# Kernel tuning notes

Hardware: AMD Instinct MI355X
Metric: run time of the kernel (lower is better)

Reference implementation:

```python
import jax, jax.numpy as jnp
import numpy as np

B, T = 32768, 32
OBJ_V, PRED_V = 179, 46
E_OBJ, E_PRED, H = 5, 5, 32
IN_DIM = E_OBJ + E_PRED + 2 + 4  # 16, matches LSTMCell input size


def setup_inputs() -> dict:
    key = jax.random.key(0)
    ks = jax.random.split(key, 12)
    s = 0.1
    return {
        "input_objects": jax.random.randint(ks[0], (B, T), 0, OBJ_V),
        "input_boxes": jax.random.uniform(ks[1], (B, T, 4), dtype=jnp.float32),
        "predicates": jax.random.randint(ks[2], (B, T), 0, PRED_V),
        "subject_indicators": jax.random.randint(ks[3], (B, T), 0, 2),
        "target_object": jax.random.randint(ks[4], (B,), 0, OBJ_V),
        "obj_emb": jax.random.normal(ks[5], (OBJ_V, E_OBJ), dtype=jnp.float32) * s,
        "pred_emb": jax.random.normal(ks[6], (PRED_V, E_PRED), dtype=jnp.float32) * s,
        "W_ih": jax.random.normal(ks[7], (4 * H, IN_DIM), dtype=jnp.float32) * s,
        "W_hh": jax.random.normal(ks[8], (4 * H, H), dtype=jnp.float32) * s,
        "b_ih": jnp.zeros((4 * H,), dtype=jnp.float32),
        "b_hh": jnp.zeros((4 * H,), dtype=jnp.float32),
        "fc2_W": jax.random.normal(ks[9], (4, H), dtype=jnp.float32) * s,
        "fc2_b": jnp.zeros((4,), dtype=jnp.float32),
    }


def _forward(input_objects, input_boxes, predicates, subject_indicators,
             obj_emb, pred_emb, W_ih, W_hh, b_ih, b_hh, fc2_W, fc2_b):
    # concatenate_features, vectorized over all timesteps at once: [B,T,16]
    feats = jnp.concatenate([
        obj_emb[input_objects],                                   # [B,T,5]
        pred_emb[predicates],                                     # [B,T,5]
        jax.nn.one_hot(subject_indicators, 2, dtype=jnp.float32), # [B,T,2]
        input_boxes,                                              # [B,T,4]
    ], axis=-1)
    xs = jnp.transpose(feats, (1, 0, 2))  # [T,B,16] for scan over time

    def step(carry, x):
        h, c = carry
        gates = x @ W_ih.T + b_ih + h @ W_hh.T + b_hh  # [B,4H]
        i, f, g, o = jnp.split(gates, 4, axis=-1)      # torch gate order i,f,g,o
        i = jax.nn.sigmoid(i)
        f = jax.nn.sigmoid(f)
        g = jnp.tanh(g)
        o = jax.nn.sigmoid(o)
        c = f * c + i * g
        h = o * jnp.tanh(c)
        return (h, c), None

    h0 = jnp.zeros((input_objects.shape[0], H), dtype=jnp.float32)
    (h, _), _ = jax.lax.scan(step, (h0, h0), xs)
    out = h @ fc2_W.T + fc2_b          # output_fc2 on last hidden state
    return jnp.clip(out, 0.0, 1.0)     # torch.clamp(min=0, max=1)


def reference(input_objects, input_boxes, predicates, subject_indicators, target_object,
              obj_emb, pred_emb, W_ih, W_hh, b_ih, b_hh, fc2_W, fc2_b):
    # target_object is accepted by the torch forward but unused in its body
    return _forward(input_objects, input_boxes, predicates, subject_indicators,
                    obj_emb, pred_emb, W_ih, W_hh, b_ih, b_hh, fc2_W, fc2_b)
```

## Files before the change

### kernel.cpp

```cpp
#include <hip/hip_runtime.h>

#define LDS_BYTES 17952

typedef _Float16 f16x8 __attribute__((ext_vector_type(8)));
typedef float    f32x4 __attribute__((ext_vector_type(4)));

#define LOG2E     1.44269504088896f
#define TWO_LOG2E 2.88539008177793f

__device__ __forceinline__ float sig_pre(float a) {
    return __builtin_amdgcn_rcpf(1.0f + __builtin_amdgcn_exp2f(a));
}
__device__ __forceinline__ float tanh_pre(float a) {
    return 1.0f - 2.0f * __builtin_amdgcn_rcpf(1.0f + __builtin_amdgcn_exp2f(a));
}

__global__ __launch_bounds__(64, 2)
void lstm_fused(const int* __restrict__ objs,
                const float* __restrict__ boxes,
                const int* __restrict__ preds,
                const int* __restrict__ subj,
                const float* __restrict__ obj_emb,
                const float* __restrict__ pred_emb,
                const float* __restrict__ W_ih,
                const float* __restrict__ W_hh,
                const float* __restrict__ b_ih,
                const float* __restrict__ b_hh,
                const float* __restrict__ fc2_W,
                const float* __restrict__ fc2_b,
                float* __restrict__ out)
{
    extern __shared__ char smem[];
    const int tid  = threadIdx.x;
    const int quad = tid >> 4;
    const int cidx = tid & 15;
    const int XOFF = 0, HOFF = 16640, ZOFF = 17920;

    {
        int* z = (int*)(smem + HOFF);
        #pragma unroll
        for (int i = 0; i < 6; ++i) {
            int idx = tid + i * 64;
            if (idx < 328) z[idx] = 0;
        }
    }

    {
        int b  = tid >> 2;
        int t0 = (tid & 3) << 3;
        long gb = (long)blockIdx.x * 16 + b;
        const int* op = objs  + gb * 32 + t0;
        const int* pp = preds + gb * 32 + t0;
        const int* sp = subj  + gb * 32 + t0;
        #pragma unroll
        for (int c = 0; c < 8; c += 4) {
            int4 ov = *(const int4*)(op + c);
            int4 pv = *(const int4*)(pp + c);
            int4 sv = *(const int4*)(sp + c);
            int oarr[4] = {ov.x, ov.y, ov.z, ov.w};
            int parr[4] = {pv.x, pv.y, pv.z, pv.w};
            int sarr[4] = {sv.x, sv.y, sv.z, sv.w};
            #pragma unroll
            for (int tt = 0; tt < 4; ++tt) {
                int t = t0 + c + tt;
                const float* eo = obj_emb  + oarr[tt] * 5;
                const float* ep = pred_emb + parr[tt] * 5;
                float4 bx = *(const float4*)(boxes + (gb * 32 + t) * 4);
                f16x8 lo, hi;
                lo[0]=(_Float16)eo[0]; lo[1]=(_Float16)eo[1]; lo[2]=(_Float16)eo[2];
                lo[3]=(_Float16)eo[3]; lo[4]=(_Float16)eo[4];
                lo[5]=(_Float16)ep[0]; lo[6]=(_Float16)ep[1]; lo[7]=(_Float16)ep[2];
                hi[0]=(_Float16)ep[3]; hi[1]=(_Float16)ep[4];
                hi[2]=(_Float16)(sarr[tt]==0 ? 1.0f : 0.0f);
                hi[3]=(_Float16)(sarr[tt]==1 ? 1.0f : 0.0f);
                hi[4]=(_Float16)bx.x; hi[5]=(_Float16)bx.y;
                hi[6]=(_Float16)bx.z; hi[7]=(_Float16)bx.w;
                char* dst = smem + XOFF + b * 1040 + t * 32;
                *(f16x8*)dst        = lo;
                *(f16x8*)(dst + 16) = hi;
            }
        }
    }

    f16x8 Wf[8][2];
    f32x4 bias4[8];
    #pragma unroll
    for (int j = 0; j < 8; ++j) {
        int n = j * 16 + cidx;
        float scale = (j >= 4 && j < 6) ? TWO_LOG2E : -LOG2E;
        float bv = (b_ih[n] + b_hh[n]) * scale;
        bias4[j] = (f32x4){bv, bv, bv, bv};
        #pragma unroll
        for (int ks = 0; ks < 2; ++ks) {
            f16x8 v;
            #pragma unroll
            for (int jj = 0; jj < 8; ++jj) {
                int k = ks * 32 + quad * 8 + jj;
                float val = (k < 16) ? W_ih[n * 16 + k]
                          : (k < 48) ? W_hh[n * 32 + (k - 16)]
                          : 0.0f;
                v[jj] = (_Float16)(val * scale);
            }
            Wf[j][ks] = v;
        }
    }

    const bool isx  = (quad < 2);
    int addr0 = isx ? (XOFF + cidx * 1040 + quad * 16)
                    : (HOFF + cidx * 80 + (quad - 2) * 16);
    const int inc0  = isx ? 32 : 0;
    const int addr1 = isx ? (HOFF + cidx * 80 + 32 + quad * 16)
                          : ZOFF;
    const int wr_b  = quad * 4;

    float cst[8] = {0,0,0,0,0,0,0,0};
    float hl[8];

    __syncthreads();

    #pragma unroll 4
    for (int t = 0; t < 32; ++t) {
        f16x8 a0 = *(const f16x8*)(smem + addr0);
        f16x8 a1 = *(const f16x8*)(smem + addr1);
        addr0 += inc0;

        f32x4 acc[8];
        #pragma unroll
        for (int j = 0; j < 8; ++j) {
            f32x4 a = __builtin_amdgcn_mfma_f32_16x16x32_f16(a0, Wf[j][0], bias4[j], 0, 0, 0);
            acc[j]  = __builtin_amdgcn_mfma_f32_16x16x32_f16(a1, Wf[j][1], a, 0, 0, 0);
        }

        #pragma unroll
        for (int r = 0; r < 4; ++r) {
            float si0 = sig_pre(acc[0][r]);
            float si1 = sig_pre(acc[1][r]);
            float sf0 = sig_pre(acc[2][r]);
            float sf1 = sig_pre(acc[3][r]);
            float tg0 = tanh_pre(acc[4][r]);
            float tg1 = tanh_pre(acc[5][r]);
            float so0 = sig_pre(acc[6][r]);
            float so1 = sig_pre(acc[7][r]);
            float c0 = fmaf(sf0, cst[2*r],   si0 * tg0);
            float c1 = fmaf(sf1, cst[2*r+1], si1 * tg1);
            cst[2*r] = c0; cst[2*r+1] = c1;
            float h0 = so0 * tanh_pre(c0 * TWO_LOG2E);
            float h1 = so1 * tanh_pre(c1 * TWO_LOG2E);
            hl[2*r] = h0; hl[2*r+1] = h1;
            *(_Float16*)(smem + HOFF + (wr_b + r) * 80 + cidx * 2)      = (_Float16)h0;
            *(_Float16*)(smem + HOFF + (wr_b + r) * 80 + 32 + cidx * 2) = (_Float16)h1;
        }
    }

    __syncthreads();
    #pragma unroll
    for (int r = 0; r < 4; ++r) {
        *(float*)(smem + (wr_b + r) * 144 + cidx * 4)      = hl[2*r];
        *(float*)(smem + (wr_b + r) * 144 + 64 + cidx * 4) = hl[2*r+1];
    }
    __syncthreads();

    {
        int b = tid >> 2, jj = tid & 3;
        const float* fw   = fc2_W + jj * 32;
        const float* hrow = (const float*)(smem + b * 144);
        float s = fc2_b[jj];
        #pragma unroll
        for (int k = 0; k < 8; ++k) {
            float4 hv = *(const float4*)(hrow + k * 4);
            s += fw[k*4+0] * hv.x + fw[k*4+1] * hv.y
               + fw[k*4+2] * hv.z + fw[k*4+3] * hv.w;
        }
        s = fminf(fmaxf(s, 0.0f), 1.0f);
        out[(long)blockIdx.x * 64 + tid] = s;
    }
}

extern "C" void kernel_launch(void* const* d_in, const int* in_sizes, int n_in,
                              void* d_out, int out_size, void* d_ws, size_t ws_size,
                              hipStream_t stream)
{
    lstm_fused<<<2048, 64, LDS_BYTES, stream>>>(
        (const int*)d_in[0], (const float*)d_in[1], (const int*)d_in[2],
        (const int*)d_in[3],
        (const float*)d_in[5], (const float*)d_in[6],
        (const float*)d_in[7], (const float*)d_in[8],
        (const float*)d_in[9], (const float*)d_in[10],
        (const float*)d_in[11], (const float*)d_in[12],
        (float*)d_out);
}
```

Baseline: 154.8 us.

## Pass hidden state via ds_bpermute and precompute input-gate MFMA one step ahead

The recurrent LSTM loop no longer round-trips the hidden state through LDS. Each step packs h into fp16 pairs and redistributes them across lanes with ds_bpermute, with the MFMA operands swapped (W as A, activations as B) so the output layout matches. The input-projection MFMA for step t+1 is issued right after the gate math, off the h-dependent critical path, and the recurrent step needs only one MFMA per gate block instead of two. This adds eight bpermutes per step and some selects, and changes the K layout of the weights.

```diff
diff --git a/kernel.cpp b/kernel.cpp
--- a/kernel.cpp
+++ b/kernel.cpp
@@ -1,6 +1,6 @@
 #include <hip/hip_runtime.h>
 
-#define LDS_BYTES 17952
+#define LDS_BYTES 16656
 
 typedef _Float16 f16x8 __attribute__((ext_vector_type(8)));
 typedef float    f32x4 __attribute__((ext_vector_type(4)));
@@ -13,6 +13,11 @@
 }
 __device__ __forceinline__ float tanh_pre(float a) {
     return 1.0f - 2.0f * __builtin_amdgcn_rcpf(1.0f + __builtin_amdgcn_exp2f(a));
+}
+__device__ __forceinline__ int pack2(float a, float b) {
+    union { _Float16 h[2]; int i; } u;
+    u.h[0] = (_Float16)a; u.h[1] = (_Float16)b;
+    return u.i;
 }
 
 __global__ __launch_bounds__(64, 2)
@@ -34,16 +39,9 @@
     const int tid  = threadIdx.x;
     const int quad = tid >> 4;
     const int cidx = tid & 15;
-    const int XOFF = 0, HOFF = 16640, ZOFF = 17920;
-
-    {
-        int* z = (int*)(smem + HOFF);
-        #pragma unroll
-        for (int i = 0; i < 6; ++i) {
-            int idx = tid + i * 64;
-            if (idx < 328) z[idx] = 0;
-        }
-    }
+    const int XOFF = 0, ZOFF = 16640;
+
+    if (tid < 4) ((int*)(smem + ZOFF))[tid] = 0;
 
     {
         int b  = tid >> 2;
@@ -86,10 +84,8 @@
     f32x4 bias4[8];
     #pragma unroll
     for (int j = 0; j < 8; ++j) {
+        float scale = (j == 4 || j == 5) ? TWO_LOG2E : -LOG2E;
         int n = j * 16 + cidx;
-        float scale = (j >= 4 && j < 6) ? TWO_LOG2E : -LOG2E;
-        float bv = (b_ih[n] + b_hh[n]) * scale;
-        bias4[j] = (f32x4){bv, bv, bv, bv};
         #pragma unroll
         for (int ks = 0; ks < 2; ++ks) {
             f16x8 v;
@@ -97,39 +93,59 @@
             for (int jj = 0; jj < 8; ++jj) {
                 int k = ks * 32 + quad * 8 + jj;
                 float val = (k < 16) ? W_ih[n * 16 + k]
-                          : (k < 48) ? W_hh[n * 32 + (k - 16)]
+                          : (k >= 32) ? W_hh[n * 32 + (k - 32)]
                           : 0.0f;
                 v[jj] = (_Float16)(val * scale);
             }
             Wf[j][ks] = v;
         }
-    }
-
-    const bool isx  = (quad < 2);
-    int addr0 = isx ? (XOFF + cidx * 1040 + quad * 16)
-                    : (HOFF + cidx * 80 + (quad - 2) * 16);
-    const int inc0  = isx ? 32 : 0;
-    const int addr1 = isx ? (HOFF + cidx * 80 + 32 + quad * 16)
-                          : ZOFF;
-    const int wr_b  = quad * 4;
-
+        #pragma unroll
+        for (int r = 0; r < 4; ++r) {
+            int nr = j * 16 + quad * 4 + r;
+            bias4[j][r] = (b_ih[nr] + b_hh[nr]) * scale;
+        }
+    }
+
+    const bool qlow = (quad < 2);
+    int       xaddr = qlow ? (XOFF + cidx * 1040 + quad * 16) : ZOFF;
+    const int xinc  = qlow ? 32 : 0;
+    const int idx_lo = (((quad & 1) << 5) + cidx) << 2;
+    const int idx_hi = idx_lo + 64;
+
+    __syncthreads();
+
+    f16x8 xfrag = *(const f16x8*)(smem + xaddr); xaddr += xinc;
+    f32x4 accp[8];
+    #pragma unroll
+    for (int j = 0; j < 8; ++j)
+        accp[j] = __builtin_amdgcn_mfma_f32_16x16x32_f16(Wf[j][0], xfrag, bias4[j], 0, 0, 0);
+
+    int pkA = 0, pkB = 0, pkC = 0, pkD = 0;
     float cst[8] = {0,0,0,0,0,0,0,0};
     float hl[8];
 
-    __syncthreads();
-
     #pragma unroll 4
     for (int t = 0; t < 32; ++t) {
-        f16x8 a0 = *(const f16x8*)(smem + addr0);
-        f16x8 a1 = *(const f16x8*)(smem + addr1);
-        addr0 += inc0;
+        int pa_lo = __builtin_amdgcn_ds_bpermute(idx_lo, pkA);
+        int pb_lo = __builtin_amdgcn_ds_bpermute(idx_lo, pkB);
+        int pa_hi = __builtin_amdgcn_ds_bpermute(idx_hi, pkA);
+        int pb_hi = __builtin_amdgcn_ds_bpermute(idx_hi, pkB);
+        int pc_lo = __builtin_amdgcn_ds_bpermute(idx_lo, pkC);
+        int pd_lo = __builtin_amdgcn_ds_bpermute(idx_lo, pkD);
+        int pc_hi = __builtin_amdgcn_ds_bpermute(idx_hi, pkC);
+        int pd_hi = __builtin_amdgcn_ds_bpermute(idx_hi, pkD);
+        union { int i[4]; f16x8 v; } hf;
+        hf.i[0] = qlow ? pa_lo : pc_lo;
+        hf.i[1] = qlow ? pb_lo : pd_lo;
+        hf.i[2] = qlow ? pa_hi : pc_hi;
+        hf.i[3] = qlow ? pb_hi : pd_hi;
 
         f32x4 acc[8];
         #pragma unroll
-        for (int j = 0; j < 8; ++j) {
-            f32x4 a = __builtin_amdgcn_mfma_f32_16x16x32_f16(a0, Wf[j][0], bias4[j], 0, 0, 0);
-            acc[j]  = __builtin_amdgcn_mfma_f32_16x16x32_f16(a1, Wf[j][1], a, 0, 0, 0);
-        }
+        for (int j = 0; j < 8; ++j)
+            acc[j] = __builtin_amdgcn_mfma_f32_16x16x32_f16(Wf[j][1], hf.v, accp[j], 0, 0, 0);
+
+        f16x8 xn = *(const f16x8*)(smem + xaddr); xaddr += xinc;
 
         #pragma unroll
         for (int r = 0; r < 4; ++r) {
@@ -144,19 +160,24 @@
             float c0 = fmaf(sf0, cst[2*r],   si0 * tg0);
             float c1 = fmaf(sf1, cst[2*r+1], si1 * tg1);
             cst[2*r] = c0; cst[2*r+1] = c1;
-            float h0 = so0 * tanh_pre(c0 * TWO_LOG2E);
-            float h1 = so1 * tanh_pre(c1 * TWO_LOG2E);
-            hl[2*r] = h0; hl[2*r+1] = h1;
-            *(_Float16*)(smem + HOFF + (wr_b + r) * 80 + cidx * 2)      = (_Float16)h0;
-            *(_Float16*)(smem + HOFF + (wr_b + r) * 80 + 32 + cidx * 2) = (_Float16)h1;
-        }
+            hl[2*r]   = so0 * tanh_pre(c0 * TWO_LOG2E);
+            hl[2*r+1] = so1 * tanh_pre(c1 * TWO_LOG2E);
+        }
+        pkA = pack2(hl[0], hl[2]);
+        pkB = pack2(hl[4], hl[6]);
+        pkC = pack2(hl[1], hl[3]);
+        pkD = pack2(hl[5], hl[7]);
+
+        #pragma unroll
+        for (int j = 0; j < 8; ++j)
+            accp[j] = __builtin_amdgcn_mfma_f32_16x16x32_f16(Wf[j][0], xn, bias4[j], 0, 0, 0);
     }
 
     __syncthreads();
     #pragma unroll
     for (int r = 0; r < 4; ++r) {
-        *(float*)(smem + (wr_b + r) * 144 + cidx * 4)      = hl[2*r];
-        *(float*)(smem + (wr_b + r) * 144 + 64 + cidx * 4) = hl[2*r+1];
+        *(float*)(smem + cidx * 144 + (quad * 4 + r) * 4)        = hl[2*r];
+        *(float*)(smem + cidx * 144 + (16 + quad * 4 + r) * 4)   = hl[2*r+1];
     }
     __syncthreads();
 
```

Result: faster. 146.0 us (-5.7%).
